# Optimization experiments

Measured on AMD Instinct MI355X. Metric: run time of the kernel, lower is better.

## Reference

```python
import jax, jax.numpy as jnp
import numpy as np
from jax import lax

B, C_IN, H, W = 128, 3, 32, 32
HC, HHC, P, NCLS = 32, 128, 4, 10
STEPS_PER_PIECE = 1           # fixed-step RK4: 1 step per unit-length piece
DT = 1.0 / STEPS_PER_PIECE
DIMNUMS = ('NCHW', 'OIHW', 'NCHW')


def setup_inputs() -> dict:
    key = jax.random.key(0)
    ks = jax.random.split(key, 8)
    def rn(k, shape, fan_in):
        return jax.random.normal(k, shape, jnp.float32) / np.sqrt(fan_in).astype(np.float32)
    return {
        'x': jax.random.normal(ks[0], (B, C_IN, H, W), jnp.float32),
        'y': jax.random.randint(ks[1], (B,), 0, NCLS),
        'aug_W': rn(ks[2], (HC, C_IN), C_IN),
        'aug_b': jnp.zeros((HC,), jnp.float32),
        'W1': rn(ks[3], (P, HHC, 1 + HC), 1 + HC),      # stacked 1x1 conv weights per piece
        'b1': jnp.zeros((P, HHC), jnp.float32),
        'W2': rn(ks[4], (P, HHC, HHC, 3, 3), HHC * 9),  # stacked 3x3 conv weights per piece
        'b2': jnp.zeros((P, HHC), jnp.float32),
        'W3': rn(ks[5], (P, HC, HHC), HHC),             # stacked 1x1 conv weights per piece
        'b3': jnp.zeros((P, HC), jnp.float32),
        'ro_W': rn(ks[6], (NCLS, HC * H * W), HC * H * W),
        'ro_b': jnp.zeros((NCLS,), jnp.float32),
    }


def _func(t, z, W1, b1, W2, b2, W3, b3):
    # piece selection: bisect(range(P+1), t) - 1, clipped -> floor(t) clipped to [0, P-1]
    idx = jnp.clip(jnp.floor(t).astype(jnp.int32), 0, P - 1)
    w1, v1 = W1[idx], b1[idx]
    w2, v2 = W2[idx], b2[idx]
    w3, v3 = W3[idx], b3[idx]
    # broadcast time as an extra channel and concat: [B, 1+HC, H, W]
    tc = jnp.full((z.shape[0], 1, z.shape[2], z.shape[3]), t, z.dtype)
    h = jnp.concatenate([tc, z], axis=1)
    h = jax.nn.softplus(jnp.einsum('bchw,oc->bohw', h, w1) + v1[:, None, None])
    h = lax.conv_general_dilated(h, w2, (1, 1), 'SAME', dimension_numbers=DIMNUMS)
    h = jax.nn.softplus(h + v2[None, :, None, None])
    h = jnp.einsum('bchw,oc->bohw', h, w3) + v3[:, None, None]
    return jnp.tanh(h)  # tanh=True


def reference(x, y, aug_W, aug_b, W1, b1, W2, b2, W3, b3, ro_W, ro_b):
    # augment: Linear over channel dim (transpose(1,3) trick == 1x1 conv)
    z = jnp.einsum('bchw,oc->bohw', x, aug_W) + aug_b[:, None, None]

    def f(t, zz):
        return _func(t, zz, W1, b1, W2, b2, W3, b3)

    dt = jnp.float32(DT)
    t0s = jnp.arange(P * STEPS_PER_PIECE, dtype=jnp.float32) * dt

    def rk4_step(zz, t0):
        k1 = f(t0, zz)
        k2 = f(t0 + dt / 2, zz + (dt / 2) * k1)
        k3 = f(t0 + dt / 2, zz + (dt / 2) * k2)
        k4 = f(t0 + dt, zz + dt * k3)
        return zz + (dt / 6) * (k1 + 2 * k2 + 2 * k3 + k4), None

    zT, _ = lax.scan(rk4_step, z, t0s)

    logits = zT.reshape(zT.shape[0], -1) @ ro_W.T + ro_b
    logp = jax.nn.log_softmax(logits, axis=-1)
    loss = -jnp.mean(jnp.take_along_axis(logp, y[:, None], axis=1))
    accuracy = (jnp.argmax(logits, axis=1) == y).sum().astype(logits.dtype)
    return loss, accuracy
```

## Files before the change

### kernel.cpp

```cpp
#include <hip/hip_runtime.h>
#include <hip/hip_bf16.h>
#include <math.h>

#define BN   128
#define CIN  3
#define HCn  32
#define HHCn 128
#define NPX  1024
#define PN   4
#define NCLS 10

#define PPAD  204
#define PPADR 208
#define PLROW 8
#define PLSZ  1664
#define H2P   136

typedef short bf16x8 __attribute__((ext_vector_type(8)));
typedef float f32x4  __attribute__((ext_vector_type(4)));

__device__ __forceinline__ float softplus_f(float x) {
    return fmaxf(x, 0.f) + __logf(1.f + __expf(-fabsf(x)));
}
__device__ __forceinline__ float tanh_fast(float x) {
    float e = __expf(-2.f * fabsf(x));
    float r = 1.f - 2.f * e * __builtin_amdgcn_rcpf(1.f + e);
    unsigned u = (__float_as_uint(r) & 0x7fffffffu) | (__float_as_uint(x) & 0x80000000u);
    return __uint_as_float(u);
}
__device__ __forceinline__ unsigned int f2bf(float f) {
    unsigned int u = __float_as_uint(f);
    return (u + 0x7fffu + ((u >> 16) & 1u)) >> 16;
}
__device__ __forceinline__ float bf2f(unsigned int h) {
    return __uint_as_float(h << 16);
}
__device__ __forceinline__ void pack2(float a, float b, unsigned int& hi, unsigned int& lo) {
    __hip_bfloat162 h2 = __float22bfloat162_rn(float2{a, b});
    unsigned int h = *reinterpret_cast<unsigned int*>(&h2);
    float ha = __uint_as_float(h << 16);
    float hb = __uint_as_float(h & 0xffff0000u);
    __hip_bfloat162 l2 = __float22bfloat162_rn(float2{a - ha, b - hb});
    hi = h;
    lo = *reinterpret_cast<unsigned int*>(&l2);
}

__global__ __launch_bounds__(256) void k_aug(
    const float* __restrict__ x, const float* __restrict__ aW,
    const float* __restrict__ ab, float* __restrict__ z)
{
    const int b = blockIdx.x, tid = threadIdx.x;
    const size_t xb = (size_t)b * CIN * NPX;
    const size_t zb = (size_t)b * HCn * NPX;
    float xv[CIN][4];
#pragma unroll
    for (int c = 0; c < CIN; c++)
#pragma unroll
        for (int j = 0; j < 4; j++)
            xv[c][j] = x[xb + c * NPX + tid + 256 * j];
    for (int o = 0; o < HCn; o++) {
        float w0 = aW[o * 3], w1 = aW[o * 3 + 1], w2 = aW[o * 3 + 2], bb = ab[o];
#pragma unroll
        for (int j = 0; j < 4; j++) {
            float v = fmaf(w0, xv[0][j], fmaf(w1, xv[1][j], fmaf(w2, xv[2][j], bb)));
            z[zb + (size_t)o * NPX + tid + 256 * j] = v;
        }
    }
}

__global__ __launch_bounds__(256) void k_packW2(
    const float* __restrict__ W2, unsigned short* __restrict__ whi,
    unsigned short* __restrict__ wlo)
{
    int t = blockIdx.x * 256 + threadIdx.x;
    int j    = t & 7;
    int lane = (t >> 3) & 63;
    int ocg  = (t >> 9) & 7;
    int kc   = (t >> 12) & 3;
    int p9s  = t >> 14;
    int sh = p9s % 9, p = p9s / 9;
    int dy = sh / 3, dx = sh % 3;
    int oc = ocg * 16 + (lane & 15);
    int ic = kc * 32 + (lane >> 4) * 8 + j;
    float v = W2[((((size_t)p * HHCn + oc) * HHCn + ic) * 3 + dy) * 3 + dx];
    unsigned int hi = f2bf(v);
    whi[t] = (unsigned short)hi;
    wlo[t] = (unsigned short)f2bf(v - bf2f(hi));
}

__global__ __launch_bounds__(256) void k_packW1(
    const float* __restrict__ W1, unsigned short* __restrict__ whi,
    unsigned short* __restrict__ wlo)
{
    int t = blockIdx.x * 256 + threadIdx.x;
    int j = t & 7, lane = (t >> 3) & 63, m = (t >> 9) & 1, kc = (t >> 10) & 3, p = t >> 12;
    int oc = kc * 32 + m * 16 + (lane & 15);
    int ic = (lane >> 4) * 8 + j;
    float v = W1[((size_t)p * HHCn + oc) * 33 + 1 + ic];
    unsigned int hi = f2bf(v);
    whi[t] = (unsigned short)hi;
    wlo[t] = (unsigned short)f2bf(v - bf2f(hi));
}

__global__ __launch_bounds__(256) void k_packW3(
    const float* __restrict__ W3, unsigned short* __restrict__ whi,
    unsigned short* __restrict__ wlo)
{
    int t = blockIdx.x * 256 + threadIdx.x;
    int j = t & 7, lane = (t >> 3) & 63, kk = (t >> 9) & 3, m = (t >> 11) & 1, p = t >> 12;
    int st = m * 16 + (lane & 15);
    int ic = kk * 32 + (lane >> 4) * 8 + j;
    float v = W3[((size_t)p * HCn + st) * HHCn + ic];
    unsigned int hi = f2bf(v);
    whi[t] = (unsigned short)hi;
    wlo[t] = (unsigned short)f2bf(v - bf2f(hi));
}

__global__ __launch_bounds__(512, 4) void k_fused(
    const float* __restrict__ z_in, const float* __restrict__ kb_in, float alpha,
    const float* __restrict__ b1p, const float* __restrict__ W1t, float t,
    const unsigned short* __restrict__ w1h, const unsigned short* __restrict__ w1l,
    const unsigned short* __restrict__ w2h, const unsigned short* __restrict__ w2l,
    const float* __restrict__ b2p,
    const unsigned short* __restrict__ w3h, const unsigned short* __restrict__ w3l,
    const float* __restrict__ b3p,
    float* __restrict__ kb_out, float* __restrict__ accb, float* __restrict__ z_out,
    int mode)
{
    const int strip = blockIdx.x, b = blockIdx.y;
    const int tid = threadIdx.x, lane = tid & 63, wid = tid >> 6;
    const int ln15 = lane & 15, lg = lane >> 4;
    const int kl8 = lg * 8, kl4 = lg * 4;

    __shared__ __align__(16) unsigned short S[39936];
    unsigned short* zinh = S;
    unsigned short* zinl = S + 6656;
    unsigned short* xh0  = S + 13312;
    unsigned short* xl0  = S + 19968;
    unsigned short* xh1  = S + 26624;
    unsigned short* xl1  = S + 33280;
    unsigned short* h2qh = S;
    unsigned short* h2ql = S + 8704;

    const size_t zbB = (size_t)b * HCn * NPX;
    const int strip0 = strip * 4;

    {
        const int ic0 = wid * 4;
        const int pl  = wid >> 1;
        const int sl  = (wid & 1) * 4;
#pragma unroll
        for (int it = 0; it < 4; it++) {
            int ppad = it * 64 + lane;
            int prow = ppad / 34, pcol = ppad - prow * 34;
            int gy = strip0 + prow - 1, gx = pcol - 1;
            bool okm = (ppad < PPAD) && (gy >= 0) && (gy < 32) && (gx >= 0) && (gx < 32);
            int gsrc = gy * 32 + gx;
            float v[4];
#pragma unroll
            for (int c = 0; c < 4; c++)
                v[c] = okm ? z_in[zbB + (size_t)(ic0 + c) * NPX + gsrc] : 0.f;
            if (alpha != 0.f) {
#pragma unroll
                for (int c = 0; c < 4; c++)
                    if (okm) v[c] = fmaf(alpha, kb_in[zbB + (size_t)(ic0 + c) * NPX + gsrc], v[c]);
            }
            unsigned int h01, l01, h23, l23;
            pack2(v[0], v[1], h01, l01);
            pack2(v[2], v[3], h23, l23);
            if (ppad < PPADR) {
                int off = pl * PLSZ + ppad * PLROW + sl;
                *(uint2*)(zinh + off) = make_uint2(h01, h23);
                *(uint2*)(zinl + off) = make_uint2(l01, l23);
            }
        }
    }

    const int wocg = (wid & 3) * 2;
    const int wph  = (wid >> 2) * 64;
    int boff[4];
#pragma unroll
    for (int f = 0; f < 4; f++) {
        int pxl = wph + f * 16 + ln15;
        boff[f] = lg * PLSZ + ((pxl >> 5) * 34 + (pxl & 31)) * PLROW;
    }

    f32x4 acc[2][4];
#pragma unroll
    for (int o = 0; o < 2; o++)
#pragma unroll
        for (int f = 0; f < 4; f++) acc[o][f] = (f32x4)(0.f);

    f32x4 c1[2][2];

    auto do_conv1 = [&](int kc) {
        const unsigned short* w1hb = w1h + (size_t)kc * 1024 + lane * 8;
        const unsigned short* w1lb = w1l + (size_t)kc * 1024 + lane * 8;
        bf16x8 a1h0 = *(const bf16x8*)w1hb, a1h1 = *(const bf16x8*)(w1hb + 512);
        bf16x8 a1l0 = *(const bf16x8*)w1lb, a1l1 = *(const bf16x8*)(w1lb + 512);
#pragma unroll
        for (int m = 0; m < 2; m++)
#pragma unroll
            for (int ni = 0; ni < 2; ni++) c1[m][ni] = (f32x4)(0.f);
#pragma unroll
        for (int ni = 0; ni < 2; ni++) {
            int n = wid + 8 * ni;
            if (ni == 0 || wid < 5) {
                int roff = lg * PLSZ + (n * 16 + ln15) * PLROW;
                bf16x8 bh = *(const bf16x8*)(zinh + roff);
                bf16x8 bl = *(const bf16x8*)(zinl + roff);
                c1[0][ni] = __builtin_amdgcn_mfma_f32_16x16x32_bf16(a1h0, bh, c1[0][ni], 0, 0, 0);
                c1[0][ni] = __builtin_amdgcn_mfma_f32_16x16x32_bf16(a1h0, bl, c1[0][ni], 0, 0, 0);
                c1[0][ni] = __builtin_amdgcn_mfma_f32_16x16x32_bf16(a1l0, bh, c1[0][ni], 0, 0, 0);
                c1[1][ni] = __builtin_amdgcn_mfma_f32_16x16x32_bf16(a1h1, bh, c1[1][ni], 0, 0, 0);
                c1[1][ni] = __builtin_amdgcn_mfma_f32_16x16x32_bf16(a1h1, bl, c1[1][ni], 0, 0, 0);
                c1[1][ni] = __builtin_amdgcn_mfma_f32_16x16x32_bf16(a1l1, bh, c1[1][ni], 0, 0, 0);
            }
        }
    };

    auto do_writeX = [&](int kc, unsigned short* xh_, unsigned short* xl_) {
        float eb[2][4];
#pragma unroll
        for (int m = 0; m < 2; m++)
#pragma unroll
            for (int r = 0; r < 4; r++) {
                int oc = kc * 32 + m * 16 + kl4 + r;
                eb[m][r] = b1p[oc] + t * W1t[oc * 33];
            }
#pragma unroll
        for (int ni = 0; ni < 2; ni++) {
            int n = wid + 8 * ni;
            if (ni == 0 || wid < 5) {
                int ppad = n * 16 + ln15;
                int prow = ppad / 34, pcol = ppad - prow * 34;
                int gy = strip0 + prow - 1;
                bool zero = (pcol == 0) || (pcol == 33) || (gy < 0) || (gy >= 32);
#pragma unroll
                for (int m = 0; m < 2; m++) {
                    float v[4];
#pragma unroll
                    for (int r = 0; r < 4; r++)
                        v[r] = zero ? 0.f : softplus_f(c1[m][ni][r] + eb[m][r]);
                    unsigned int h01, l01, h23, l23;
                    pack2(v[0], v[1], h01, l01);
                    pack2(v[2], v[3], h23, l23);
                    int off = (m * 2 + (kl4 >> 3)) * PLSZ + ppad * PLROW + (kl4 & 7);
                    *(uint2*)(xh_ + off) = make_uint2(h01, h23);
                    *(uint2*)(xl_ + off) = make_uint2(l01, l23);
                }
            }
        }
    };

    auto do_conv3 = [&](int kc, const unsigned short* xh_, const unsigned short* xl_) {
#pragma unroll
        for (int sh = 0; sh < 9; sh++) {
            const size_t wbase = ((size_t)(sh * 4 + kc) * 8 + wocg) * 512 + lane * 8;
            bf16x8 ah0 = *(const bf16x8*)(w2h + wbase);
            bf16x8 al0 = *(const bf16x8*)(w2l + wbase);
            bf16x8 ah1 = *(const bf16x8*)(w2h + wbase + 512);
            bf16x8 al1 = *(const bf16x8*)(w2l + wbase + 512);
            const int soff = ((sh / 3) * 34 + (sh % 3)) * PLROW;
#pragma unroll
            for (int f = 0; f < 4; f++) {
                bf16x8 bh = *(const bf16x8*)(xh_ + boff[f] + soff);
                bf16x8 bl = *(const bf16x8*)(xl_ + boff[f] + soff);
                acc[0][f] = __builtin_amdgcn_mfma_f32_16x16x32_bf16(ah0, bh, acc[0][f], 0, 0, 0);
                acc[0][f] = __builtin_amdgcn_mfma_f32_16x16x32_bf16(ah0, bl, acc[0][f], 0, 0, 0);
                acc[0][f] = __builtin_amdgcn_mfma_f32_16x16x32_bf16(al0, bh, acc[0][f], 0, 0, 0);
                acc[1][f] = __builtin_amdgcn_mfma_f32_16x16x32_bf16(ah1, bh, acc[1][f], 0, 0, 0);
                acc[1][f] = __builtin_amdgcn_mfma_f32_16x16x32_bf16(ah1, bl, acc[1][f], 0, 0, 0);
                acc[1][f] = __builtin_amdgcn_mfma_f32_16x16x32_bf16(al1, bh, acc[1][f], 0, 0, 0);
            }
        }
    };

    __syncthreads();
    do_conv1(0);
    do_writeX(0, xh0, xl0);
    __syncthreads();

    do_conv1(1); do_writeX(1, xh1, xl1); do_conv3(0, xh0, xl0);
    __syncthreads();
    do_conv1(2); do_writeX(2, xh0, xl0); do_conv3(1, xh1, xl1);
    __syncthreads();
    do_conv1(3); do_writeX(3, xh1, xl1); do_conv3(2, xh0, xl0);
    __syncthreads();
    do_conv3(3, xh1, xl1);

    float bb2[2][4];
#pragma unroll
    for (int o2 = 0; o2 < 2; o2++)
#pragma unroll
        for (int r = 0; r < 4; r++)
            bb2[o2][r] = b2p[(wocg + o2) * 16 + kl4 + r];

    const size_t obB = (size_t)b * HCn * NPX + strip * 128;
    const int m3 = wid & 1, n4 = wid >> 1;
    float bb3[4];
#pragma unroll
    for (int r = 0; r < 4; r++) bb3[r] = b3p[m3 * 16 + kl4 + r];

#pragma unroll
    for (int q = 0; q < 2; q++) {
        __syncthreads();
        if ((wid >> 2) == q) {
#pragma unroll
            for (int o2 = 0; o2 < 2; o2++)
#pragma unroll
                for (int f2 = 0; f2 < 4; f2++) {
                    f32x4 a = acc[o2][f2];
                    float v[4];
#pragma unroll
                    for (int r = 0; r < 4; r++) v[r] = softplus_f(a[r] + bb2[o2][r]);
                    unsigned int h01, l01, h23, l23;
                    pack2(v[0], v[1], h01, l01);
                    pack2(v[2], v[3], h23, l23);
                    int off = (f2 * 16 + ln15) * H2P + (wocg + o2) * 16 + kl4;
                    *(uint2*)(h2qh + off) = make_uint2(h01, h23);
                    *(uint2*)(h2ql + off) = make_uint2(l01, l23);
                }
        }
        __syncthreads();
        f32x4 c3 = (f32x4)(0.f);
#pragma unroll
        for (int kk = 0; kk < 4; kk++) {
            const unsigned short* a3hb = w3h + (size_t)(m3 * 4 + kk) * 512 + lane * 8;
            const unsigned short* a3lb = w3l + (size_t)(m3 * 4 + kk) * 512 + lane * 8;
            bf16x8 a3h = *(const bf16x8*)a3hb;
            bf16x8 a3l = *(const bf16x8*)a3lb;
            bf16x8 bh = *(const bf16x8*)(h2qh + (n4 * 16 + ln15) * H2P + kk * 32 + kl8);
            bf16x8 bl = *(const bf16x8*)(h2ql + (n4 * 16 + ln15) * H2P + kk * 32 + kl8);
            c3 = __builtin_amdgcn_mfma_f32_16x16x32_bf16(a3h, bh, c3, 0, 0, 0);
            c3 = __builtin_amdgcn_mfma_f32_16x16x32_bf16(a3h, bl, c3, 0, 0, 0);
            c3 = __builtin_amdgcn_mfma_f32_16x16x32_bf16(a3l, bh, c3, 0, 0, 0);
        }
#pragma unroll
        for (int r = 0; r < 4; r++) {
            int st = m3 * 16 + kl4 + r;
            float v = tanh_fast(c3[r] + bb3[r]);
            size_t i = obB + (size_t)st * NPX + q * 64 + n4 * 16 + ln15;
            if (mode == 0)      { kb_out[i] = v; accb[i] = v; }
            else if (mode == 1) { kb_out[i] = v; accb[i] += 2.f * v; }
            else                { z_out[i] = z_in[i] + (accb[i] + v) * (1.f / 6.f); }
        }
    }
}

__global__ __launch_bounds__(256) void k_logits(
    const float* __restrict__ z, const float* __restrict__ roW,
    const float* __restrict__ rob, float* __restrict__ logits)
{
    const int b = blockIdx.x, tid = threadIdx.x;
    float p[NCLS];
#pragma unroll
    for (int c = 0; c < NCLS; c++) p[c] = 0.f;
    const float* zp = z + (size_t)b * 32768;
    for (int i = tid; i < 32768; i += 256) {
        float zv = zp[i];
#pragma unroll
        for (int c = 0; c < NCLS; c++) p[c] = fmaf(zv, roW[(size_t)c * 32768 + i], p[c]);
    }
#pragma unroll
    for (int c = 0; c < NCLS; c++)
        for (int off = 32; off > 0; off >>= 1) p[c] += __shfl_down(p[c], off, 64);
    __shared__ float red[4][NCLS];
    int wid = tid >> 6, lane = tid & 63;
    if (lane == 0)
#pragma unroll
        for (int c = 0; c < NCLS; c++) red[wid][c] = p[c];
    __syncthreads();
    if (tid < NCLS) {
        float s = red[0][tid] + red[1][tid] + red[2][tid] + red[3][tid] + rob[tid];
        logits[b * NCLS + tid] = s;
    }
}

__global__ __launch_bounds__(128) void k_loss(
    const float* __restrict__ logits, const int* __restrict__ y,
    float* __restrict__ out)
{
    const int b = threadIdx.x;
    float l[NCLS];
#pragma unroll
    for (int c = 0; c < NCLS; c++) l[c] = logits[b * NCLS + c];
    float m = l[0]; int am = 0;
#pragma unroll
    for (int c = 1; c < NCLS; c++) if (l[c] > m) { m = l[c]; am = c; }
    float s = 0.f;
#pragma unroll
    for (int c = 0; c < NCLS; c++) s += expf(l[c] - m);
    float lse = m + logf(s);
    int yy = y[b];
    float loss_b = lse - l[yy];
    float corr = (am == yy) ? 1.f : 0.f;
    for (int off = 32; off > 0; off >>= 1) {
        loss_b += __shfl_down(loss_b, off, 64);
        corr   += __shfl_down(corr,   off, 64);
    }
    __shared__ float sl[2], sc[2];
    if ((b & 63) == 0) { sl[b >> 6] = loss_b; sc[b >> 6] = corr; }
    __syncthreads();
    if (b == 0) {
        out[0] = (sl[0] + sl[1]) / (float)BN;
        out[1] = sc[0] + sc[1];
    }
}

extern "C" void kernel_launch(void* const* d_in, const int* in_sizes, int n_in,
                              void* d_out, int out_size, void* d_ws, size_t ws_size,
                              hipStream_t stream) {
    const float* x   = (const float*)d_in[0];
    const int*   y   = (const int*)  d_in[1];
    const float* aW  = (const float*)d_in[2];
    const float* ab  = (const float*)d_in[3];
    const float* W1  = (const float*)d_in[4];
    const float* b1  = (const float*)d_in[5];
    const float* W2  = (const float*)d_in[6];
    const float* b2  = (const float*)d_in[7];
    const float* W3  = (const float*)d_in[8];
    const float* b3  = (const float*)d_in[9];
    const float* roW = (const float*)d_in[10];
    const float* rob = (const float*)d_in[11];
    float* out = (float*)d_out;
    float* ws  = (float*)d_ws;

    const size_t ZSZ = (size_t)BN * HCn * NPX;
    float* zb0    = ws;
    float* zb1    = zb0 + ZSZ;
    float* kb0    = zb1 + ZSZ;
    float* kb1    = kb0 + ZSZ;
    float* accb   = kb1 + ZSZ;
    float* logits = accb + ZSZ;
    unsigned short* w2h = (unsigned short*)(logits + 4096);
    unsigned short* w2l = w2h + 589824;
    unsigned short* w1h = w2l + 589824;
    unsigned short* w1l = w1h + 16384;
    unsigned short* w3h = w1l + 16384;
    unsigned short* w3l = w3h + 16384;

    k_packW2<<<2304, 256, 0, stream>>>(W2, w2h, w2l);
    k_packW1<<<64, 256, 0, stream>>>(W1, w1h, w1l);
    k_packW3<<<64, 256, 0, stream>>>(W3, w3h, w3l);
    k_aug<<<BN, 256, 0, stream>>>(x, aW, ab, zb0);

    float* zA = zb0;
    float* zB = zb1;
    for (int p = 0; p < PN; p++) {
        for (int e = 0; e < 4; e++) {
            const int idx = (e == 3 && p + 1 < PN) ? p + 1 : p;
            const float t = (float)p + (e == 0 ? 0.f : (e == 3 ? 1.f : 0.5f));
            const float alpha = (e == 0) ? 0.f : (e == 3 ? 1.f : 0.5f);
            const int mode = (e == 0) ? 0 : (e == 3 ? 2 : 1);
            const float* kbin = (e == 2) ? kb1 : kb0;
            float* kbout = (e == 1) ? kb1 : kb0;
            k_fused<<<dim3(8, BN), 512, 0, stream>>>(
                zA, kbin, alpha,
                b1 + (size_t)idx * HHCn, W1 + (size_t)idx * HHCn * 33, t,
                w1h + (size_t)idx * 4096, w1l + (size_t)idx * 4096,
                w2h + (size_t)idx * 147456, w2l + (size_t)idx * 147456,
                b2 + (size_t)idx * HHCn,
                w3h + (size_t)idx * 4096, w3l + (size_t)idx * 4096,
                b3 + (size_t)idx * HCn,
                kbout, accb, zB, mode);
        }
        float* tmp = zA; zA = zB; zB = tmp;
    }

    k_logits<<<BN, 256, 0, stream>>>(zA, roW, rob, logits);
    k_loss<<<1, 128, 0, stream>>>(logits, y, out);
}
```

Before: 1.992 ms.

## Emit next stage input pre-packed as padded bf16 hi/lo planes

Each fused RK stage now computes the next stage's input (z + alpha*k) in its epilogue and writes it as split bf16 hi/lo in a zero-padded, LDS-ready layout. The following stage loads its halo strip with plain 16-byte copies and no longer gathers fp32 z and k, does the fma, or packs. The kb buffers go away. The cost is extra padded global buffers, a memset, and a per-stage read of z_in in the epilogue.

```diff
diff --git a/kernel.cpp b/kernel.cpp
--- a/kernel.cpp
+++ b/kernel.cpp
@@ -10,11 +10,12 @@
 #define PN   4
 #define NCLS 10
 
-#define PPAD  204
-#define PPADR 208
 #define PLROW 8
 #define PLSZ  1664
 #define H2P   136
+
+#define PGPU  9728
+#define IMGU  77824
 
 typedef short bf16x8 __attribute__((ext_vector_type(8)));
 typedef float f32x4  __attribute__((ext_vector_type(4)));
@@ -47,23 +48,44 @@
 
 __global__ __launch_bounds__(256) void k_aug(
     const float* __restrict__ x, const float* __restrict__ aW,
-    const float* __restrict__ ab, float* __restrict__ z)
+    const float* __restrict__ ab, float* __restrict__ z,
+    unsigned short* __restrict__ pz0)
 {
     const int b = blockIdx.x, tid = threadIdx.x;
     const size_t xb = (size_t)b * CIN * NPX;
     const size_t zb = (size_t)b * HCn * NPX;
+    unsigned short* pzi = pz0 + (size_t)b * IMGU;
     float xv[CIN][4];
 #pragma unroll
     for (int c = 0; c < CIN; c++)
 #pragma unroll
         for (int j = 0; j < 4; j++)
             xv[c][j] = x[xb + c * NPX + tid + 256 * j];
-    for (int o = 0; o < HCn; o++) {
-        float w0 = aW[o * 3], w1 = aW[o * 3 + 1], w2 = aW[o * 3 + 2], bb = ab[o];
+#pragma unroll
+    for (int plane = 0; plane < 4; plane++) {
+        float v[8][4];
+#pragma unroll
+        for (int s = 0; s < 8; s++) {
+            int o = plane * 8 + s;
+            float w0 = aW[o * 3], w1 = aW[o * 3 + 1], w2 = aW[o * 3 + 2], bb = ab[o];
+#pragma unroll
+            for (int j = 0; j < 4; j++) {
+                float vv = fmaf(w0, xv[0][j], fmaf(w1, xv[1][j], fmaf(w2, xv[2][j], bb)));
+                v[s][j] = vv;
+                z[zb + (size_t)o * NPX + tid + 256 * j] = vv;
+            }
+        }
 #pragma unroll
         for (int j = 0; j < 4; j++) {
-            float v = fmaf(w0, xv[0][j], fmaf(w1, xv[1][j], fmaf(w2, xv[2][j], bb)));
-            z[zb + (size_t)o * NPX + tid + 256 * j] = v;
+            int pix = tid + 256 * j;
+            int row = ((pix >> 5) + 1) * 34 + (pix & 31) + 1;
+            unsigned int h01, l01, h23, l23, h45, l45, h67, l67;
+            pack2(v[0][j], v[1][j], h01, l01);
+            pack2(v[2][j], v[3][j], h23, l23);
+            pack2(v[4][j], v[5][j], h45, l45);
+            pack2(v[6][j], v[7][j], h67, l67);
+            *(uint4*)(pzi + (size_t)plane * PGPU + row * 8) = make_uint4(h01, h23, h45, h67);
+            *(uint4*)(pzi + (size_t)(4 + plane) * PGPU + row * 8) = make_uint4(l01, l23, l45, l67);
         }
     }
 }
@@ -117,15 +139,15 @@
 }
 
 __global__ __launch_bounds__(512, 4) void k_fused(
-    const float* __restrict__ z_in, const float* __restrict__ kb_in, float alpha,
+    const float* __restrict__ z_in, const unsigned short* __restrict__ pz_in,
     const float* __restrict__ b1p, const float* __restrict__ W1t, float t,
     const unsigned short* __restrict__ w1h, const unsigned short* __restrict__ w1l,
     const unsigned short* __restrict__ w2h, const unsigned short* __restrict__ w2l,
     const float* __restrict__ b2p,
     const unsigned short* __restrict__ w3h, const unsigned short* __restrict__ w3l,
     const float* __restrict__ b3p,
-    float* __restrict__ kb_out, float* __restrict__ accb, float* __restrict__ z_out,
-    int mode)
+    float* __restrict__ accb, float* __restrict__ z_out,
+    unsigned short* __restrict__ pz_out, float alpha_next, int mode)
 {
     const int strip = blockIdx.x, b = blockIdx.y;
     const int tid = threadIdx.x, lane = tid & 63, wid = tid >> 6;
@@ -142,42 +164,24 @@
     unsigned short* h2qh = S;
     unsigned short* h2ql = S + 8704;
 
-    const size_t zbB = (size_t)b * HCn * NPX;
-    const int strip0 = strip * 4;
-
     {
-        const int ic0 = wid * 4;
-        const int pl  = wid >> 1;
-        const int sl  = (wid & 1) * 4;
-#pragma unroll
-        for (int it = 0; it < 4; it++) {
-            int ppad = it * 64 + lane;
-            int prow = ppad / 34, pcol = ppad - prow * 34;
-            int gy = strip0 + prow - 1, gx = pcol - 1;
-            bool okm = (ppad < PPAD) && (gy >= 0) && (gy < 32) && (gx >= 0) && (gx < 32);
-            int gsrc = gy * 32 + gx;
-            float v[4];
-#pragma unroll
-            for (int c = 0; c < 4; c++)
-                v[c] = okm ? z_in[zbB + (size_t)(ic0 + c) * NPX + gsrc] : 0.f;
-            if (alpha != 0.f) {
-#pragma unroll
-                for (int c = 0; c < 4; c++)
-                    if (okm) v[c] = fmaf(alpha, kb_in[zbB + (size_t)(ic0 + c) * NPX + gsrc], v[c]);
-            }
-            unsigned int h01, l01, h23, l23;
-            pack2(v[0], v[1], h01, l01);
-            pack2(v[2], v[3], h23, l23);
-            if (ppad < PPADR) {
-                int off = pl * PLSZ + ppad * PLROW + sl;
-                *(uint2*)(zinh + off) = make_uint2(h01, h23);
-                *(uint2*)(zinl + off) = make_uint2(l01, l23);
+        const unsigned short* src0 = pz_in + (size_t)b * IMGU;
+        const int rowoff = strip * 136;
+#pragma unroll
+        for (int i = 0; i < 4; i++) {
+            int c = tid + 512 * i;
+            if (c < 1664) {
+                int region = c / 208;
+                int row = c - region * 208;
+                uint4 d = *(const uint4*)(src0 + (size_t)region * PGPU + (size_t)(rowoff + row) * 8);
+                *(uint4*)(S + region * 1664 + row * 8) = d;
             }
         }
     }
 
     const int wocg = (wid & 3) * 2;
     const int wph  = (wid >> 2) * 64;
+    const int strip0 = strip * 4;
     int boff[4];
 #pragma unroll
     for (int f = 0; f < 4; f++) {
@@ -336,15 +340,27 @@
             c3 = __builtin_amdgcn_mfma_f32_16x16x32_bf16(a3h, bl, c3, 0, 0, 0);
             c3 = __builtin_amdgcn_mfma_f32_16x16x32_bf16(a3l, bh, c3, 0, 0, 0);
         }
+        const int st0 = m3 * 16 + kl4;
+        const int pix = strip * 128 + q * 64 + n4 * 16 + ln15;
+        const int prow_g = ((pix >> 5) + 1) * 34 + (pix & 31) + 1;
+        float pk[4];
 #pragma unroll
         for (int r = 0; r < 4; r++) {
-            int st = m3 * 16 + kl4 + r;
+            int st = st0 + r;
             float v = tanh_fast(c3[r] + bb3[r]);
             size_t i = obB + (size_t)st * NPX + q * 64 + n4 * 16 + ln15;
-            if (mode == 0)      { kb_out[i] = v; accb[i] = v; }
-            else if (mode == 1) { kb_out[i] = v; accb[i] += 2.f * v; }
-            else                { z_out[i] = z_in[i] + (accb[i] + v) * (1.f / 6.f); }
-        }
+            float zv = z_in[i];
+            if (mode == 0)      { accb[i] = v;           pk[r] = fmaf(alpha_next, v, zv); }
+            else if (mode == 1) { accb[i] += 2.f * v;    pk[r] = fmaf(alpha_next, v, zv); }
+            else { float zn = zv + (accb[i] + v) * (1.f / 6.f); z_out[i] = zn; pk[r] = zn; }
+        }
+        unsigned int h01, l01, h23, l23;
+        pack2(pk[0], pk[1], h01, l01);
+        pack2(pk[2], pk[3], h23, l23);
+        unsigned short* dsth = pz_out + (size_t)b * IMGU + (size_t)(st0 >> 3) * PGPU
+                               + (size_t)prow_g * 8 + (st0 & 7);
+        *(uint2*)dsth = make_uint2(h01, h23);
+        *(uint2*)(dsth + (size_t)4 * PGPU) = make_uint2(l01, l23);
     }
 }
 
@@ -429,9 +445,7 @@
     const size_t ZSZ = (size_t)BN * HCn * NPX;
     float* zb0    = ws;
     float* zb1    = zb0 + ZSZ;
-    float* kb0    = zb1 + ZSZ;
-    float* kb1    = kb0 + ZSZ;
-    float* accb   = kb1 + ZSZ;
+    float* accb   = zb1 + ZSZ;
     float* logits = accb + ZSZ;
     unsigned short* w2h = (unsigned short*)(logits + 4096);
     unsigned short* w2l = w2h + 589824;
@@ -439,33 +453,37 @@
     unsigned short* w1l = w1h + 16384;
     unsigned short* w3h = w1l + 16384;
     unsigned short* w3l = w3h + 16384;
+    unsigned short* pz0 = w3l + 16384;
+    unsigned short* pz1 = pz0 + (size_t)BN * IMGU;
+
+    hipMemsetAsync(pz0, 0, (size_t)2 * BN * IMGU * sizeof(unsigned short), stream);
 
     k_packW2<<<2304, 256, 0, stream>>>(W2, w2h, w2l);
     k_packW1<<<64, 256, 0, stream>>>(W1, w1h, w1l);
     k_packW3<<<64, 256, 0, stream>>>(W3, w3h, w3l);
-    k_aug<<<BN, 256, 0, stream>>>(x, aW, ab, zb0);
+    k_aug<<<BN, 256, 0, stream>>>(x, aW, ab, zb0, pz0);
 
     float* zA = zb0;
     float* zB = zb1;
-    for (int p = 0; p < PN; p++) {
-        for (int e = 0; e < 4; e++) {
-            const int idx = (e == 3 && p + 1 < PN) ? p + 1 : p;
-            const float t = (float)p + (e == 0 ? 0.f : (e == 3 ? 1.f : 0.5f));
-            const float alpha = (e == 0) ? 0.f : (e == 3 ? 1.f : 0.5f);
-            const int mode = (e == 0) ? 0 : (e == 3 ? 2 : 1);
-            const float* kbin = (e == 2) ? kb1 : kb0;
-            float* kbout = (e == 1) ? kb1 : kb0;
-            k_fused<<<dim3(8, BN), 512, 0, stream>>>(
-                zA, kbin, alpha,
-                b1 + (size_t)idx * HHCn, W1 + (size_t)idx * HHCn * 33, t,
-                w1h + (size_t)idx * 4096, w1l + (size_t)idx * 4096,
-                w2h + (size_t)idx * 147456, w2l + (size_t)idx * 147456,
-                b2 + (size_t)idx * HHCn,
-                w3h + (size_t)idx * 4096, w3l + (size_t)idx * 4096,
-                b3 + (size_t)idx * HCn,
-                kbout, accb, zB, mode);
-        }
-        float* tmp = zA; zA = zB; zB = tmp;
+    unsigned short* pza = pz0;
+    unsigned short* pzb = pz1;
+    for (int ge = 0; ge < 16; ge++) {
+        const int p = ge >> 2, e = ge & 3;
+        const int idx = (e == 3 && p + 1 < PN) ? p + 1 : p;
+        const float t = (float)p + (e == 0 ? 0.f : (e == 3 ? 1.f : 0.5f));
+        const int mode = (e == 0) ? 0 : (e == 3 ? 2 : 1);
+        const float alpha_next = (e == 2) ? 1.f : ((e == 3) ? 0.f : 0.5f);
+        k_fused<<<dim3(8, BN), 512, 0, stream>>>(
+            zA, pza,
+            b1 + (size_t)idx * HHCn, W1 + (size_t)idx * HHCn * 33, t,
+            w1h + (size_t)idx * 4096, w1l + (size_t)idx * 4096,
+            w2h + (size_t)idx * 147456, w2l + (size_t)idx * 147456,
+            b2 + (size_t)idx * HHCn,
+            w3h + (size_t)idx * 4096, w3l + (size_t)idx * 4096,
+            b3 + (size_t)idx * HCn,
+            accb, zB, pzb, alpha_next, mode);
+        unsigned short* tp = pza; pza = pzb; pzb = tp;
+        if (e == 3) { float* tz = zA; zA = zB; zB = tz; }
     }
 
     k_logits<<<BN, 256, 0, stream>>>(zA, roW, rob, logits);
```

After: 1.947 ms (median of 2 runs). 2.3% less time.
